# Kernel tuning notes

Hardware: AMD Instinct MI355X
Metric: run time of the kernel (lower is better)

Reference implementation:

```python
import jax, jax.numpy as jnp
import numpy as np

N_DATA = 131072
N_HID = 32768
D = 256
E1 = 524288  # data -> hidden
E2 = 524288  # hidden -> hidden
E3 = 524288  # hidden -> data


def setup_inputs() -> dict:
    key = jax.random.key(0)
    ks = jax.random.split(key, 32)
    rn = lambda k, shape, s=0.05: (jax.random.normal(k, shape, jnp.float32) * s)
    inp = {
        "data_x": jax.random.normal(ks[0], (N_DATA, 8), jnp.float32),
        "hidden_x": jax.random.normal(ks[1], (N_HID, 3), jnp.float32),
        "dh_src": jax.random.randint(ks[2], (E1,), 0, N_DATA, jnp.int32),
        "dh_dst": jax.random.randint(ks[3], (E1,), 0, N_HID, jnp.int32),
        "hh_src": jax.random.randint(ks[4], (E2,), 0, N_HID, jnp.int32),
        "hh_dst": jax.random.randint(ks[5], (E2,), 0, N_HID, jnp.int32),
        "hd_src": jax.random.randint(ks[6], (E3,), 0, N_HID, jnp.int32),
        "hd_dst": jax.random.randint(ks[7], (E3,), 0, N_DATA, jnp.int32),
        # encoder params
        "enc_src_w": rn(ks[8], (D, 8)), "enc_src_b": rn(ks[9], (D,)),
        "enc_dst_w": rn(ks[10], (D, 3)), "enc_dst_b": rn(ks[11], (D,)),
        "enc_wl": rn(ks[12], (D, D)), "enc_bl": rn(ks[13], (D,)), "enc_wr": rn(ks[14], (D, D)),
        # processor params
        "proc_wl": rn(ks[15], (D, D)), "proc_bl": rn(ks[16], (D,)), "proc_wr": rn(ks[17], (D, D)),
        "proc_mlp_w": rn(ks[18], (D, D)), "proc_mlp_b": rn(ks[19], (D,)),
        # decoder params
        "dec_src_w": rn(ks[20], (D, D)), "dec_src_b": rn(ks[21], (D,)),
        "dec_dst_w": rn(ks[22], (D, 8)), "dec_dst_b": rn(ks[23], (D,)),
        "dec_wl": rn(ks[24], (D, D)), "dec_bl": rn(ks[25], (D,)), "dec_wr": rn(ks[26], (D, D)),
        "out_w": rn(ks[27], (8, D)), "out_b": rn(ks[28], (8,)),
    }
    return inp


def _gelu(x):
    return jax.nn.gelu(x, approximate=False)  # torch nn.GELU default (erf)


def _sage(x_src, x_dst, src, dst, wl, bl, wr, n_dst):
    """PyG SAGEConv, mean aggregation: lin_l(mean_j x_src[j]) + lin_r(x_dst)."""
    msg = x_src[src]                                              # [E, D] gather
    agg = jax.ops.segment_sum(msg, dst, num_segments=n_dst)       # [n_dst, D]
    cnt = jax.ops.segment_sum(jnp.ones((src.shape[0], 1), msg.dtype), dst,
                              num_segments=n_dst)
    mean = agg / jnp.maximum(cnt, 1.0)
    return mean @ wl.T + bl + x_dst @ wr.T


def reference(data_x, hidden_x, dh_src, dh_dst, hh_src, hh_dst, hd_src, hd_dst,
              enc_src_w, enc_src_b, enc_dst_w, enc_dst_b, enc_wl, enc_bl, enc_wr,
              proc_wl, proc_bl, proc_wr, proc_mlp_w, proc_mlp_b,
              dec_src_w, dec_src_b, dec_dst_w, dec_dst_b, dec_wl, dec_bl, dec_wr,
              out_w, out_b):
    # ---- encoder: data -> hidden ----
    h_data = _gelu(data_x @ enc_src_w.T + enc_src_b)
    h_hid = _gelu(hidden_x @ enc_dst_w.T + enc_dst_b)
    h_hid = _gelu(_sage(h_data, h_hid, dh_src, dh_dst, enc_wl, enc_bl, enc_wr, N_HID))
    # ---- processor: hidden -> hidden, then GELU-Linear-GELU MLP ----
    h_hid = _sage(h_hid, h_hid, hh_src, hh_dst, proc_wl, proc_bl, proc_wr, N_HID)
    h_hid = _gelu(_gelu(h_hid) @ proc_mlp_w.T + proc_mlp_b)
    # ---- decoder: hidden -> data ----
    s = _gelu(h_hid @ dec_src_w.T + dec_src_b)
    d = _gelu(data_x @ dec_dst_w.T + dec_dst_b)
    d = _gelu(_sage(s, d, hd_src, hd_dst, dec_wl, dec_bl, dec_wr, N_DATA))
    return d @ out_w.T + out_b  # [N_DATA, 8]
```

## Files before the change

kernel.cpp:

```cpp
#include <hip/hip_runtime.h>
#include <stdint.h>

#define NDATA 131072
#define NHID  32768
#define NEDGE 524288

typedef __bf16 bf16_t;
typedef __bf16 bf16x4 __attribute__((ext_vector_type(4)));
typedef __bf16 bf16x8 __attribute__((ext_vector_type(8)));
typedef float  f32x4  __attribute__((ext_vector_type(4)));

__device__ __forceinline__ float gelu_f(float x) {
    return 0.5f * x * (1.0f + erff(x * 0.7071067811865476f));
}

__device__ __forceinline__ void glds16(const void* g, void* l) {
    auto* gp = reinterpret_cast<const __attribute__((address_space(1))) uint32_t*>(
        reinterpret_cast<uintptr_t>(g));
    auto* lp = reinterpret_cast<__attribute__((address_space(3))) uint32_t*>(
        reinterpret_cast<uintptr_t>(l));
    __builtin_amdgcn_global_load_lds(gp, lp, 16, 0, 0);
}

struct WPtrs { const float* p[9]; };

struct EdgePtrs { const int* src[3]; const int* dst[3]; };

__device__ __forceinline__ int cnt_off_of(int g) { return g == 0 ? 0 : (g == 1 ? NHID : 2 * NHID); }
__device__ __forceinline__ int rp_off_of(int g)  { return g == 0 ? 0 : (g == 1 ? NHID + 1 : 2 * NHID + 2); }
__device__ __forceinline__ int shift_of(int g)   { return g == 2 ? 10 : 8; }

__global__ __launch_bounds__(256)
void hist3(EdgePtrs ep, int* __restrict__ cnt_all) {
    const int g = blockIdx.x >> 11;
    const int i = ((blockIdx.x & 2047) << 8) + threadIdx.x;
    atomicAdd(&cnt_all[cnt_off_of(g) + ep.dst[g][i]], 1);
}

__global__ __launch_bounds__(256)
void scan_blk3(const int* __restrict__ cnt_all, int* __restrict__ pre_all,
               int* __restrict__ blk) {
    __shared__ int sh[256];
    const int bid = blockIdx.x;
    int g, local;
    if (bid < 32)      { g = 0; local = bid; }
    else if (bid < 64) { g = 1; local = bid - 32; }
    else               { g = 2; local = bid - 64; }
    const int t = threadIdx.x;
    const int cbase = cnt_off_of(g) + local * 1024 + t * 4;
    const int pbase = rp_off_of(g)  + local * 1024 + t * 4;
    int4 v = *(const int4*)(cnt_all + cbase);
    sh[t] = v.x + v.y + v.z + v.w;
    __syncthreads();
    for (int off = 1; off < 256; off <<= 1) {
        int other = 0;
        if (t >= off) other = sh[t - off];
        __syncthreads();
        if (t >= off) sh[t] += other;
        __syncthreads();
    }
    const int excl = (t == 0) ? 0 : sh[t - 1];
    int4 o;
    o.x = excl; o.y = o.x + v.x; o.z = o.y + v.y; o.w = o.z + v.z;
    *(int4*)(pre_all + pbase) = o;
    if (t == 255) blk[bid] = sh[255];
}

__global__ __launch_bounds__(256)
void scan_add3(const int* __restrict__ pre_all, const int* __restrict__ blk,
               int* __restrict__ rp_all, int* __restrict__ binA) {
    __shared__ int sh[256];
    const int bid = blockIdx.x;
    int g, local, gbase;
    if (bid < 32)      { g = 0; local = bid;      gbase = 0; }
    else if (bid < 64) { g = 1; local = bid - 32; gbase = 32; }
    else               { g = 2; local = bid - 64; gbase = 64; }
    const int t = threadIdx.x;
    int part = 0;
    if (t < local) part = blk[gbase + t];
    sh[t] = part;
    __syncthreads();
    for (int o2 = 128; o2 > 0; o2 >>= 1) {
        if (t < o2) sh[t] += sh[t + o2];
        __syncthreads();
    }
    const int off = sh[0];
    const int idx = local * 1024 + t * 4;
    const int pbase = rp_off_of(g) + idx;
    int4 v = *(const int4*)(pre_all + pbase);
    v.x += off; v.y += off; v.z += off; v.w += off;
    *(int4*)(rp_all + pbase) = v;
    const int bw = 1 << shift_of(g);
    if ((idx & (bw - 1)) == 0) binA[g * 128 + (idx >> shift_of(g))] = v.x;
    if (local == 0 && t == 0) {
        const int n = (g == 2) ? NDATA : NHID;
        rp_all[rp_off_of(g) + n] = NEDGE;
    }
}

__global__ __launch_bounds__(256)
void partition3(EdgePtrs ep, int* __restrict__ binA, int2* __restrict__ pairs) {
    __shared__ int hist[128], base[128], cur[128];
    const int g = blockIdx.x >> 7;
    const int blk = blockIdx.x & 127;
    const int t = threadIdx.x;
    const int shift = shift_of(g);
    const int e_base = blk * 4096;
    const int* src = ep.src[g];
    const int* dst = ep.dst[g];
    if (t < 128) { hist[t] = 0; cur[t] = 0; }
    __syncthreads();
    #pragma unroll
    for (int it = 0; it < 16; ++it) {
        const int d = dst[e_base + it * 256 + t];
        atomicAdd(&hist[d >> shift], 1);
    }
    __syncthreads();
    if (t < 128) base[t] = atomicAdd(&binA[g * 128 + t], hist[t]);
    __syncthreads();
    #pragma unroll
    for (int it = 0; it < 16; ++it) {
        const int e = e_base + it * 256 + t;
        const int s = src[e], d = dst[e];
        const int b = d >> shift;
        const int l = atomicAdd(&cur[b], 1);
        pairs[(size_t)g * NEDGE + base[b] + l] = make_int2(s, d);
    }
}

__global__ __launch_bounds__(256)
void binsort3(const int2* __restrict__ pairs, const int* __restrict__ rp_all,
              int* __restrict__ sorted_all) {
    __shared__ int cur[1024];
    const int g = blockIdx.x >> 7;
    const int b = blockIdx.x & 127;
    const int t = threadIdx.x;
    const int shift = shift_of(g);
    const int W = 1 << shift;
    const int d0 = b << shift;
    const int rpo = rp_off_of(g);
    for (int i = t; i < W; i += 256) cur[i] = rp_all[rpo + d0 + i];
    __syncthreads();
    const int e0 = rp_all[rpo + d0];
    const int e1 = rp_all[rpo + d0 + W];
    for (int e = e0 + t; e < e1; e += 256) {
        const int2 p = pairs[(size_t)g * NEDGE + e];
        const int pos = atomicAdd(&cur[p.y - d0], 1);
        sorted_all[(size_t)g * NEDGE + pos] = p.x;
    }
}

__global__ __launch_bounds__(256)
void csr_gather_mean(const bf16_t* __restrict__ feat, const int* __restrict__ row_ptr,
                     const int* __restrict__ sorted_src, bf16_t* __restrict__ mean, int n) {
    const int lane = threadIdx.x & 63;
    const int half = lane >> 5;
    const int col8 = (lane & 31) * 8;
    const int w = blockIdx.x * 4 + (threadIdx.x >> 6);
    if (w >= n) return;
    const int e0 = row_ptr[w], e1 = row_ptr[w + 1];
    float acc[8] = {0.f, 0.f, 0.f, 0.f, 0.f, 0.f, 0.f, 0.f};
    int e = e0 + half;
    for (; e + 6 < e1; e += 8) {
        const int s0 = sorted_src[e],     s1 = sorted_src[e + 2];
        const int s2 = sorted_src[e + 4], s3 = sorted_src[e + 6];
        const bf16x8 v0 = *(const bf16x8*)(feat + (size_t)s0 * 256 + col8);
        const bf16x8 v1 = *(const bf16x8*)(feat + (size_t)s1 * 256 + col8);
        const bf16x8 v2 = *(const bf16x8*)(feat + (size_t)s2 * 256 + col8);
        const bf16x8 v3 = *(const bf16x8*)(feat + (size_t)s3 * 256 + col8);
        #pragma unroll
        for (int j = 0; j < 8; ++j)
            acc[j] += ((float)v0[j] + (float)v1[j]) + ((float)v2[j] + (float)v3[j]);
    }
    for (; e < e1; e += 2) {
        const int s0 = sorted_src[e];
        const bf16x8 v0 = *(const bf16x8*)(feat + (size_t)s0 * 256 + col8);
        #pragma unroll
        for (int j = 0; j < 8; ++j) acc[j] += (float)v0[j];
    }
    #pragma unroll
    for (int j = 0; j < 8; ++j) acc[j] += __shfl_xor(acc[j], 32, 64);
    if (half == 0) {
        const float ic = 1.0f / fmaxf((float)(e1 - e0), 1.0f);
        bf16x8 r;
        #pragma unroll
        for (int j = 0; j < 8; ++j) r[j] = (bf16_t)(acc[j] * ic);
        *(bf16x8*)(mean + (size_t)w * 256 + col8) = r;
    }
}

__global__ __launch_bounds__(256)
void enc_cvt_both(WPtrs wp, bf16_t* __restrict__ wout,
                  const float* __restrict__ hx, const float* __restrict__ w3,
                  const float* __restrict__ b3, bf16_t* __restrict__ out3,
                  const float* __restrict__ dx, const float* __restrict__ w8,
                  const float* __restrict__ b8, bf16_t* __restrict__ out8) {
    __shared__ float ws[8 * 256];
    __shared__ float bs[256];
    const int t = threadIdx.x;
    if (blockIdx.x < 2056) {
        const int i = blockIdx.x * 256 + t;
        if (i < 8 * 65536) {
            const int wsel = i >> 16, off = i & 65535;
            wout[i] = (bf16_t)wp.p[wsel][off];
        } else {
            wout[i] = (bf16_t)wp.p[8][i - 8 * 65536];
        }
        return;
    }
    const int bid = blockIdx.x - 2056;
    const bool is8 = (bid >= 512);
    if (is8) {
        #pragma unroll
        for (int j = 0; j < 8; ++j) ws[j * 256 + t] = w8[t * 8 + j];
        bs[t] = b8[t];
    } else {
        #pragma unroll
        for (int j = 0; j < 3; ++j) ws[j * 256 + t] = w3[t * 3 + j];
        bs[t] = b3[t];
    }
    __syncthreads();
    const int lane = t & 63, wv = t >> 6;
    const int f0 = lane * 4;
    const float4 b4 = *(const float4*)(&bs[f0]);
    if (!is8) {
        for (int node = bid * 4 + wv; node < NHID; node += 512 * 4) {
            const float* xr = hx + (size_t)node * 3;
            float xv[3];
            #pragma unroll
            for (int j = 0; j < 3; ++j) xv[j] = xr[j];
            float a0 = b4.x, a1 = b4.y, a2 = b4.z, a3 = b4.w;
            #pragma unroll
            for (int j = 0; j < 3; ++j) {
                const float4 w4 = *(const float4*)(&ws[j * 256 + f0]);
                a0 += xv[j] * w4.x; a1 += xv[j] * w4.y;
                a2 += xv[j] * w4.z; a3 += xv[j] * w4.w;
            }
            bf16x4 r;
            r[0] = (bf16_t)gelu_f(a0); r[1] = (bf16_t)gelu_f(a1);
            r[2] = (bf16_t)gelu_f(a2); r[3] = (bf16_t)gelu_f(a3);
            *(bf16x4*)(out3 + (size_t)node * 256 + f0) = r;
        }
    } else {
        for (int node = (bid - 512) * 4 + wv; node < NDATA; node += 2048 * 4) {
            const float* xr = dx + (size_t)node * 8;
            float xv[8];
            #pragma unroll
            for (int j = 0; j < 8; ++j) xv[j] = xr[j];
            float a0 = b4.x, a1 = b4.y, a2 = b4.z, a3 = b4.w;
            #pragma unroll
            for (int j = 0; j < 8; ++j) {
                const float4 w4 = *(const float4*)(&ws[j * 256 + f0]);
                a0 += xv[j] * w4.x; a1 += xv[j] * w4.y;
                a2 += xv[j] * w4.z; a3 += xv[j] * w4.w;
            }
            bf16x4 r;
            r[0] = (bf16_t)gelu_f(a0); r[1] = (bf16_t)gelu_f(a1);
            r[2] = (bf16_t)gelu_f(a2); r[3] = (bf16_t)gelu_f(a3);
            *(bf16x4*)(out8 + (size_t)node * 256 + f0) = r;
        }
    }
}

template<int DUAL, int ACT>
__global__ __launch_bounds__(256)
void mfma_gemm(const bf16_t* __restrict__ A1, const bf16_t* __restrict__ W1,
               const bf16_t* __restrict__ A2, const bf16_t* __restrict__ W2,
               const float* __restrict__ bias, bf16_t* __restrict__ C) {
    __shared__ bf16_t As[4 * 64 * 8];
    __shared__ bf16_t Bs[4 * 128 * 8];
    const int t = threadIdx.x;
    const int w = t >> 6, lane = t & 63;
    const int l15 = lane & 15, l4 = lane >> 4;
    const int m0 = (blockIdx.x >> 1) * 64;
    const int n0 = (blockIdx.x & 1) * 128;

    f32x4 acc[4][2];
    #pragma unroll
    for (int nb = 0; nb < 2; ++nb) {
        const float bv = bias ? bias[n0 + w * 32 + nb * 16 + l15] : 0.0f;
        #pragma unroll
        for (int m = 0; m < 4; ++m) {
            acc[m][nb][0] = bv; acc[m][nb][1] = bv; acc[m][nb][2] = bv; acc[m][nb][3] = bv;
        }
    }

    #pragma unroll
    for (int p = 0; p <= DUAL; ++p) {
        const bf16_t* Ap = p ? A2 : A1;
        const bf16_t* Wp = p ? W2 : W1;
        for (int kt = 0; kt < 8; ++kt) {
            const int k0 = kt * 32;
            __syncthreads();
            glds16(Ap + (size_t)(m0 + lane) * 256 + k0 + w * 8, &As[(w * 64) * 8]);
            glds16(Wp + (size_t)(n0 + lane) * 256 + k0 + w * 8, &Bs[(w * 128) * 8]);
            glds16(Wp + (size_t)(n0 + 64 + lane) * 256 + k0 + w * 8, &Bs[(w * 128 + 64) * 8]);
            __syncthreads();
            bf16x8 af[4], bfr[2];
            #pragma unroll
            for (int m = 0; m < 4; ++m)
                af[m] = *(const bf16x8*)(&As[(l4 * 64 + m * 16 + l15) * 8]);
            #pragma unroll
            for (int nb = 0; nb < 2; ++nb)
                bfr[nb] = *(const bf16x8*)(&Bs[(l4 * 128 + w * 32 + nb * 16 + l15) * 8]);
            #pragma unroll
            for (int m = 0; m < 4; ++m)
                #pragma unroll
                for (int nb = 0; nb < 2; ++nb)
                    acc[m][nb] = __builtin_amdgcn_mfma_f32_16x16x32_bf16(af[m], bfr[nb], acc[m][nb], 0, 0, 0);
        }
    }

    #pragma unroll
    for (int m = 0; m < 4; ++m) {
        #pragma unroll
        for (int nb = 0; nb < 2; ++nb) {
            const int col = n0 + w * 32 + nb * 16 + l15;
            #pragma unroll
            for (int i = 0; i < 4; ++i) {
                const int row = m0 + m * 16 + l4 * 4 + i;
                const float v = acc[m][nb][i];
                C[(size_t)row * 256 + col] = (bf16_t)(ACT ? gelu_f(v) : v);
            }
        }
    }
}

__global__ __launch_bounds__(256)
void gemm_chain2(const bf16_t* __restrict__ A1, const bf16_t* __restrict__ W1,
                 const float* __restrict__ b1, const bf16_t* __restrict__ W2,
                 bf16_t* __restrict__ C) {
    __shared__ bf16_t As[4 * 64 * 8];
    __shared__ bf16_t Bs[4 * 256 * 8];
    __shared__ bf16_t sL[32 * 64 * 8];
    const int t = threadIdx.x;
    const int w = t >> 6, lane = t & 63;
    const int l15 = lane & 15, l4 = lane >> 4;
    const int m0 = blockIdx.x * 64;

    f32x4 acc[4][4];
    #pragma unroll
    for (int nb = 0; nb < 4; ++nb) {
        const float bv = b1[w * 64 + nb * 16 + l15];
        #pragma unroll
        for (int m = 0; m < 4; ++m) {
            acc[m][nb][0] = bv; acc[m][nb][1] = bv; acc[m][nb][2] = bv; acc[m][nb][3] = bv;
        }
    }

    for (int kt = 0; kt < 8; ++kt) {
        const int k0 = kt * 32;
        __syncthreads();
        glds16(A1 + (size_t)(m0 + lane) * 256 + k0 + w * 8, &As[(w * 64) * 8]);
        #pragma unroll
        for (int q = 0; q < 4; ++q)
            glds16(W1 + (size_t)(w * 64 + lane) * 256 + k0 + q * 8,
                   &Bs[(q * 256 + w * 64) * 8]);
        __syncthreads();
        bf16x8 af[4], bfr[4];
        #pragma unroll
        for (int m = 0; m < 4; ++m)
            af[m] = *(const bf16x8*)(&As[(l4 * 64 + m * 16 + l15) * 8]);
        #pragma unroll
        for (int nb = 0; nb < 4; ++nb)
            bfr[nb] = *(const bf16x8*)(&Bs[(l4 * 256 + w * 64 + nb * 16 + l15) * 8]);
        #pragma unroll
        for (int m = 0; m < 4; ++m)
            #pragma unroll
            for (int nb = 0; nb < 4; ++nb)
                acc[m][nb] = __builtin_amdgcn_mfma_f32_16x16x32_bf16(af[m], bfr[nb], acc[m][nb], 0, 0, 0);
    }
    #pragma unroll
    for (int m = 0; m < 4; ++m) {
        #pragma unroll
        for (int nb = 0; nb < 4; ++nb) {
            const int col = w * 64 + nb * 16 + l15;
            const int kq = col >> 3, cj = col & 7;
            #pragma unroll
            for (int i = 0; i < 4; ++i) {
                const int row = m * 16 + l4 * 4 + i;
                sL[(kq * 64 + row) * 8 + cj] = (bf16_t)gelu_f(acc[m][nb][i]);
            }
            acc[m][nb][0] = 0.f; acc[m][nb][1] = 0.f; acc[m][nb][2] = 0.f; acc[m][nb][3] = 0.f;
        }
    }
    __syncthreads();

    for (int kt = 0; kt < 8; ++kt) {
        const int k0 = kt * 32;
        __syncthreads();
        #pragma unroll
        for (int q = 0; q < 4; ++q)
            glds16(W2 + (size_t)(w * 64 + lane) * 256 + k0 + q * 8,
                   &Bs[(q * 256 + w * 64) * 8]);
        __syncthreads();
        bf16x8 af[4], bfr[4];
        #pragma unroll
        for (int m = 0; m < 4; ++m)
            af[m] = *(const bf16x8*)(&sL[((kt * 4 + l4) * 64 + m * 16 + l15) * 8]);
        #pragma unroll
        for (int nb = 0; nb < 4; ++nb)
            bfr[nb] = *(const bf16x8*)(&Bs[(l4 * 256 + w * 64 + nb * 16 + l15) * 8]);
        #pragma unroll
        for (int m = 0; m < 4; ++m)
            #pragma unroll
            for (int nb = 0; nb < 4; ++nb)
                acc[m][nb] = __builtin_amdgcn_mfma_f32_16x16x32_bf16(af[m], bfr[nb], acc[m][nb], 0, 0, 0);
    }

    #pragma unroll
    for (int m = 0; m < 4; ++m) {
        #pragma unroll
        for (int nb = 0; nb < 4; ++nb) {
            const int col = w * 64 + nb * 16 + l15;
            #pragma unroll
            for (int i = 0; i < 4; ++i) {
                const int row = m0 + m * 16 + l4 * 4 + i;
                C[(size_t)row * 256 + col] = (bf16_t)acc[m][nb][i];
            }
        }
    }
}

__global__ __launch_bounds__(256)
void dec_gemm_m(const bf16_t* __restrict__ A1mean,
                const float* __restrict__ xdat, const float* __restrict__ Wd,
                const float* __restrict__ bd, const bf16_t* __restrict__ W2,
                const float* __restrict__ bias, const bf16_t* __restrict__ owb,
                const float* __restrict__ ob, float* __restrict__ out) {
    __shared__ __align__(16) char smem[25600];
    bf16_t* As   = (bf16_t*)smem;
    bf16_t* Bs   = (bf16_t*)(smem + 4096);
    bf16_t* wd16 = (bf16_t*)(smem + 20480);
    float*  bdS  = (float*)(smem + 24576);
    bf16_t* tt   = (bf16_t*)smem;
    float*  part = (float*)(smem + 16384);

    const int t = threadIdx.x;
    const int w = t >> 6, lane = t & 63;
    const int l15 = lane & 15, l4 = lane >> 4;
    const int m0 = blockIdx.x * 64;

    {
        const float4 wa = *(const float4*)(Wd + t * 8);
        const float4 wb = *(const float4*)(Wd + t * 8 + 4);
        bf16x8 wv;
        wv[0] = (bf16_t)wa.x; wv[1] = (bf16_t)wa.y; wv[2] = (bf16_t)wa.z; wv[3] = (bf16_t)wa.w;
        wv[4] = (bf16_t)wb.x; wv[5] = (bf16_t)wb.y; wv[6] = (bf16_t)wb.z; wv[7] = (bf16_t)wb.w;
        *(bf16x8*)(&wd16[t * 8]) = wv;
        bdS[t] = bd[t];
    }
    bf16x8 af_x;
    #pragma unroll
    for (int j = 0; j < 8; ++j) af_x[j] = (bf16_t)0.0f;
    if (l4 == 0) {
        const float* xrp = xdat + (size_t)(m0 + w * 16 + l15) * 8;
        const float4 xa = *(const float4*)(xrp);
        const float4 xb = *(const float4*)(xrp + 4);
        af_x[0] = (bf16_t)xa.x; af_x[1] = (bf16_t)xa.y; af_x[2] = (bf16_t)xa.z; af_x[3] = (bf16_t)xa.w;
        af_x[4] = (bf16_t)xb.x; af_x[5] = (bf16_t)xb.y; af_x[6] = (bf16_t)xb.z; af_x[7] = (bf16_t)xb.w;
    }

    f32x4 acc[4][4];
    #pragma unroll
    for (int nb = 0; nb < 4; ++nb) {
        const float bv = bias[w * 64 + nb * 16 + l15];
        #pragma unroll
        for (int m = 0; m < 4; ++m) {
            acc[m][nb][0] = bv; acc[m][nb][1] = bv; acc[m][nb][2] = bv; acc[m][nb][3] = bv;
        }
    }
    {
        bf16x8 ifr[2];
        #pragma unroll
        for (int p = 0; p < 2; ++p)
            #pragma unroll
            for (int j = 0; j < 8; ++j)
                ifr[p][j] = (bf16_t)((l4 * 8 + j == p * 16 + l15) ? 1.0f : 0.0f);
        #pragma unroll
        for (int m = 0; m < 4; ++m) {
            #pragma unroll
            for (int c = 0; c < 2; ++c) {
                const bf16x8 am = *(const bf16x8*)(A1mean +
                    (size_t)(m0 + m * 16 + l15) * 256 + (2 * w + c) * 32 + l4 * 8);
                acc[m][c * 2 + 0] = __builtin_amdgcn_mfma_f32_16x16x32_bf16(am, ifr[0], acc[m][c * 2 + 0], 0, 0, 0);
                acc[m][c * 2 + 1] = __builtin_amdgcn_mfma_f32_16x16x32_bf16(am, ifr[1], acc[m][c * 2 + 1], 0, 0, 0);
            }
        }
    }
    __syncthreads();

    for (int kt = 0; kt < 8; ++kt) {
        const int k0 = kt * 32;
        __syncthreads();
        #pragma unroll
        for (int nb2 = 0; nb2 < 2; ++nb2) {
            const int cl = nb2 * 16 + l15;
            const int col = k0 + cl;
            f32x4 ad;
            const float bv = bdS[col];
            ad[0] = bv; ad[1] = bv; ad[2] = bv; ad[3] = bv;
            bf16x8 bf_d;
            #pragma unroll
            for (int j = 0; j < 8; ++j) bf_d[j] = (bf16_t)0.0f;
            if (l4 == 0) bf_d = *(const bf16x8*)(&wd16[col * 8]);
            ad = __builtin_amdgcn_mfma_f32_16x16x32_bf16(af_x, bf_d, ad, 0, 0, 0);
            const int kq = cl >> 3, jj = cl & 7;
            #pragma unroll
            for (int i = 0; i < 4; ++i)
                As[(kq * 64 + w * 16 + l4 * 4 + i) * 8 + jj] = (bf16_t)gelu_f(ad[i]);
        }
        #pragma unroll
        for (int q = 0; q < 4; ++q)
            glds16(W2 + (size_t)(w * 64 + lane) * 256 + k0 + q * 8,
                   &Bs[(q * 256 + w * 64) * 8]);
        __syncthreads();
        bf16x8 af[4], bfr[4];
        #pragma unroll
        for (int m = 0; m < 4; ++m)
            af[m] = *(const bf16x8*)(&As[(l4 * 64 + m * 16 + l15) * 8]);
        #pragma unroll
        for (int nb = 0; nb < 4; ++nb)
            bfr[nb] = *(const bf16x8*)(&Bs[(l4 * 256 + w * 64 + nb * 16 + l15) * 8]);
        #pragma unroll
        for (int m = 0; m < 4; ++m)
            #pragma unroll
            for (int nb = 0; nb < 4; ++nb)
                acc[m][nb] = __builtin_amdgcn_mfma_f32_16x16x32_bf16(af[m], bfr[nb], acc[m][nb], 0, 0, 0);
    }

    __syncthreads();

    bf16x8 owf[2];
    #pragma unroll
    for (int s = 0; s < 2; ++s) {
        #pragma unroll
        for (int j = 0; j < 8; ++j) owf[s][j] = (bf16_t)0.0f;
        if (l15 < 8)
            owf[s] = *(const bf16x8*)(owb + l15 * 256 + w * 64 + s * 32 + l4 * 8);
    }

    bf16_t* ttw = tt + w * 2048;
    #pragma unroll
    for (int h = 0; h < 2; ++h) {
        #pragma unroll
        for (int mm = 0; mm < 2; ++mm) {
            const int m = h * 2 + mm;
            #pragma unroll
            for (int nb = 0; nb < 4; ++nb) {
                const int col = nb * 16 + l15;
                const int kg = col >> 3, cj = col & 7;
                #pragma unroll
                for (int i = 0; i < 4; ++i) {
                    const int rl = mm * 16 + l4 * 4 + i;
                    ttw[(kg * 32 + rl) * 8 + cj] = (bf16_t)gelu_f(acc[m][nb][i]);
                }
            }
        }
        f32x4 accp[2];
        #pragma unroll
        for (int mb = 0; mb < 2; ++mb) {
            accp[mb][0] = 0.f; accp[mb][1] = 0.f; accp[mb][2] = 0.f; accp[mb][3] = 0.f;
            #pragma unroll
            for (int s = 0; s < 2; ++s) {
                const bf16x8 af = *(const bf16x8*)(&ttw[((s * 4 + l4) * 32 + mb * 16 + l15) * 8]);
                accp[mb] = __builtin_amdgcn_mfma_f32_16x16x32_bf16(af, owf[s], accp[mb], 0, 0, 0);
            }
        }
        __syncthreads();
        #pragma unroll
        for (int mb = 0; mb < 2; ++mb)
            #pragma unroll
            for (int i = 0; i < 4; ++i)
                part[(w * 32 + mb * 16 + l4 * 4 + i) * 16 + l15] = accp[mb][i];
        __syncthreads();
        {
            const int row = t >> 3, o = t & 7;
            const float v = part[(0 * 32 + row) * 16 + o] + part[(1 * 32 + row) * 16 + o]
                          + part[(2 * 32 + row) * 16 + o] + part[(3 * 32 + row) * 16 + o] + ob[o];
            out[(size_t)(m0 + h * 32 + row) * 8 + o] = v;
        }
    }
}


extern "C" void kernel_launch(void* const* d_in, const int* in_sizes, int n_in,
                              void* d_out, int out_size, void* d_ws, size_t ws_size,
                              hipStream_t stream) {
    const float* data_x   = (const float*)d_in[0];
    const float* hidden_x = (const float*)d_in[1];
    const int* dh_src = (const int*)d_in[2];
    const int* dh_dst = (const int*)d_in[3];
    const int* hh_src = (const int*)d_in[4];
    const int* hh_dst = (const int*)d_in[5];
    const int* hd_src = (const int*)d_in[6];
    const int* hd_dst = (const int*)d_in[7];
    const float* enc_src_w = (const float*)d_in[8];
    const float* enc_src_b = (const float*)d_in[9];
    const float* enc_dst_w = (const float*)d_in[10];
    const float* enc_dst_b = (const float*)d_in[11];
    const float* enc_wl = (const float*)d_in[12];
    const float* enc_bl = (const float*)d_in[13];
    const float* enc_wr = (const float*)d_in[14];
    const float* proc_wl = (const float*)d_in[15];
    const float* proc_bl = (const float*)d_in[16];
    const float* proc_wr = (const float*)d_in[17];
    const float* proc_mlp_w = (const float*)d_in[18];
    const float* proc_mlp_b = (const float*)d_in[19];
    const float* dec_src_w = (const float*)d_in[20];
    const float* dec_src_b = (const float*)d_in[21];
    const float* dec_dst_w = (const float*)d_in[22];
    const float* dec_dst_b = (const float*)d_in[23];
    const float* dec_wl = (const float*)d_in[24];
    const float* dec_bl = (const float*)d_in[25];
    const float* dec_wr = (const float*)d_in[26];
    const float* out_w  = (const float*)d_in[27];
    const float* out_b  = (const float*)d_in[28];
    float* out = (float*)d_out;

    bf16_t* h_a   = (bf16_t*)d_ws;
    bf16_t* h_b   = h_a + (size_t)NHID * 256;
    bf16_t* h_c   = h_b + (size_t)NHID * 256;
    bf16_t* h_msg = h_c + (size_t)NHID * 256;
    bf16_t* dmean = h_msg + (size_t)NDATA * 256;
    bf16_t* wbuf  = dmean + (size_t)NDATA * 256;
    int* cnt_all    = (int*)(wbuf + 8 * 65536 + 2048);
    int* rp_all     = cnt_all + (2 * NHID + NDATA);
    int* sorted_all = rp_all + (2 * NHID + NDATA + 3);
    int* blk_sums   = sorted_all + (size_t)3 * NEDGE;
    int* binA       = blk_sums + 192;
    int2* pairs     = (int2*)(((uintptr_t)(binA + 384) + 15) & ~(uintptr_t)15);

    bf16_t* W_enc_wl  = wbuf + 0 * 65536;
    bf16_t* W_enc_wr  = wbuf + 1 * 65536;
    bf16_t* W_proc_wl = wbuf + 2 * 65536;
    bf16_t* W_proc_wr = wbuf + 3 * 65536;
    bf16_t* W_mlp     = wbuf + 4 * 65536;
    bf16_t* W_dec_src = wbuf + 5 * 65536;
    bf16_t* W_dec_wl  = wbuf + 6 * 65536;
    bf16_t* W_dec_wr  = wbuf + 7 * 65536;
    bf16_t* W_out     = wbuf + 8 * 65536;

    const int* rp_dh = rp_all;
    const int* rp_hh = rp_all + NHID + 1;
    const int* rp_hd = rp_all + 2 * NHID + 2;
    const int* so_dh = sorted_all;
    const int* so_hh = sorted_all + NEDGE;
    const int* so_hd = sorted_all + 2 * (size_t)NEDGE;

    WPtrs wp;
    wp.p[0] = enc_wl;  wp.p[1] = enc_wr;  wp.p[2] = proc_wl; wp.p[3] = proc_wr;
    wp.p[4] = proc_mlp_w; wp.p[5] = dec_src_w; wp.p[6] = dec_wl; wp.p[7] = dec_wr;
    wp.p[8] = out_w;

    EdgePtrs ep;
    ep.src[0] = dh_src; ep.dst[0] = dh_dst;
    ep.src[1] = hh_src; ep.dst[1] = hh_dst;
    ep.src[2] = hd_src; ep.dst[2] = hd_dst;
    hipMemsetAsync(cnt_all, 0, (size_t)(2 * NHID + NDATA) * sizeof(int), stream);
    hist3<<<3 * 2048, 256, 0, stream>>>(ep, cnt_all);
    scan_blk3<<<192, 256, 0, stream>>>(cnt_all, rp_all, blk_sums);
    scan_add3<<<192, 256, 0, stream>>>(rp_all, blk_sums, rp_all, binA);
    partition3<<<3 * 128, 256, 0, stream>>>(ep, binA, pairs);
    binsort3<<<3 * 128, 256, 0, stream>>>(pairs, rp_all, sorted_all);

    enc_cvt_both<<<4616, 256, 0, stream>>>(wp, wbuf,
                                           hidden_x, enc_dst_w, enc_dst_b, h_a,
                                           data_x, enc_src_w, enc_src_b, h_msg);
    csr_gather_mean<<<NHID / 4, 256, 0, stream>>>(h_msg, rp_dh, so_dh, h_b, NHID);
    mfma_gemm<1, 1><<<(NHID / 64) * 2, 256, 0, stream>>>(h_b, W_enc_wl, h_a, W_enc_wr, enc_bl, h_c);

    csr_gather_mean<<<NHID / 4, 256, 0, stream>>>(h_c, rp_hh, so_hh, h_a, NHID);
    mfma_gemm<1, 1><<<(NHID / 64) * 2, 256, 0, stream>>>(h_a, W_proc_wl, h_c, W_proc_wr, proc_bl, h_b);
    mfma_gemm<0, 1><<<(NHID / 64) * 2, 256, 0, stream>>>(h_b, W_mlp, nullptr, nullptr, proc_mlp_b, h_a);
    gemm_chain2<<<NHID / 64, 256, 0, stream>>>(h_a, W_dec_src, dec_src_b, W_dec_wl, h_c);

    csr_gather_mean<<<NDATA / 4, 256, 0, stream>>>(h_c, rp_hd, so_hd, dmean, NDATA);
    dec_gemm_m<<<NDATA / 64, 256, 0, stream>>>(dmean, data_x, dec_dst_w, dec_dst_b,
                                               W_dec_wr, dec_bl, W_out, out_b, out);
}
```

Before: 448.3 us.

## Precompute decoder dst tile in LDS and read W2 fragments from global

Result: no change. 454.9 us (+1.5%).

```diff
diff --git a/kernel.cpp b/kernel.cpp
--- a/kernel.cpp
+++ b/kernel.cpp
@@ -22,7 +22,7 @@
     __builtin_amdgcn_global_load_lds(gp, lp, 16, 0, 0);
 }
 
-struct WPtrs { const float* p[9]; };
+struct WPtrs { const float* p[10]; };
 
 struct EdgePtrs { const int* src[3]; const int* dst[3]; };
 
@@ -198,17 +198,19 @@
     __shared__ float ws[8 * 256];
     __shared__ float bs[256];
     const int t = threadIdx.x;
-    if (blockIdx.x < 2056) {
+    if (blockIdx.x < 2064) {
         const int i = blockIdx.x * 256 + t;
         if (i < 8 * 65536) {
             const int wsel = i >> 16, off = i & 65535;
             wout[i] = (bf16_t)wp.p[wsel][off];
+        } else if (i < 8 * 65536 + 2048) {
+            wout[i] = (bf16_t)wp.p[8][i - 8 * 65536];
         } else {
-            wout[i] = (bf16_t)wp.p[8][i - 8 * 65536];
+            wout[i] = (bf16_t)wp.p[9][i - (8 * 65536 + 2048)];
         }
         return;
     }
-    const int bid = blockIdx.x - 2056;
+    const int bid = blockIdx.x - 2064;
     const bool is8 = (bid >= 512);
     if (is8) {
         #pragma unroll
@@ -424,15 +426,12 @@
 
 __global__ __launch_bounds__(256)
 void dec_gemm_m(const bf16_t* __restrict__ A1mean,
-                const float* __restrict__ xdat, const float* __restrict__ Wd,
+                const float* __restrict__ xdat, const bf16_t* __restrict__ wdb,
                 const float* __restrict__ bd, const bf16_t* __restrict__ W2,
                 const float* __restrict__ bias, const bf16_t* __restrict__ owb,
                 const float* __restrict__ ob, float* __restrict__ out) {
-    __shared__ __align__(16) char smem[25600];
-    bf16_t* As   = (bf16_t*)smem;
-    bf16_t* Bs   = (bf16_t*)(smem + 4096);
-    bf16_t* wd16 = (bf16_t*)(smem + 20480);
-    float*  bdS  = (float*)(smem + 24576);
+    __shared__ __align__(16) char smem[32768];
+    bf16_t* dL = (bf16_t*)smem;
     bf16_t* tt   = (bf16_t*)smem;
     float*  part = (float*)(smem + 16384);
 
@@ -441,15 +440,6 @@
     const int l15 = lane & 15, l4 = lane >> 4;
     const int m0 = blockIdx.x * 64;
 
-    {
-        const float4 wa = *(const float4*)(Wd + t * 8);
-        const float4 wb = *(const float4*)(Wd + t * 8 + 4);
-        bf16x8 wv;
-        wv[0] = (bf16_t)wa.x; wv[1] = (bf16_t)wa.y; wv[2] = (bf16_t)wa.z; wv[3] = (bf16_t)wa.w;
-        wv[4] = (bf16_t)wb.x; wv[5] = (bf16_t)wb.y; wv[6] = (bf16_t)wb.z; wv[7] = (bf16_t)wb.w;
-        *(bf16x8*)(&wd16[t * 8]) = wv;
-        bdS[t] = bd[t];
-    }
     bf16x8 af_x;
     #pragma unroll
     for (int j = 0; j < 8; ++j) af_x[j] = (bf16_t)0.0f;
@@ -461,6 +451,23 @@
         af_x[4] = (bf16_t)xb.x; af_x[5] = (bf16_t)xb.y; af_x[6] = (bf16_t)xb.z; af_x[7] = (bf16_t)xb.w;
     }
 
+    #pragma unroll
+    for (int cb = 0; cb < 16; ++cb) {
+        const int col = cb * 16 + l15;
+        f32x4 ad;
+        const float bv = bd[col];
+        ad[0] = bv; ad[1] = bv; ad[2] = bv; ad[3] = bv;
+        bf16x8 bf_d;
+        #pragma unroll
+        for (int j = 0; j < 8; ++j) bf_d[j] = (bf16_t)0.0f;
+        if (l4 == 0) bf_d = *(const bf16x8*)(wdb + col * 8);
+        ad = __builtin_amdgcn_mfma_f32_16x16x32_bf16(af_x, bf_d, ad, 0, 0, 0);
+        const int kq = col >> 3, jj = col & 7;
+        #pragma unroll
+        for (int i = 0; i < 4; ++i)
+            dL[(kq * 64 + w * 16 + l4 * 4 + i) * 8 + jj] = (bf16_t)gelu_f(ad[i]);
+    }
+
     f32x4 acc[4][4];
     #pragma unroll
     for (int nb = 0; nb < 4; ++nb) {
@@ -492,36 +499,14 @@
 
     for (int kt = 0; kt < 8; ++kt) {
         const int k0 = kt * 32;
-        __syncthreads();
-        #pragma unroll
-        for (int nb2 = 0; nb2 < 2; ++nb2) {
-            const int cl = nb2 * 16 + l15;
-            const int col = k0 + cl;
-            f32x4 ad;
-            const float bv = bdS[col];
-            ad[0] = bv; ad[1] = bv; ad[2] = bv; ad[3] = bv;
-            bf16x8 bf_d;
-            #pragma unroll
-            for (int j = 0; j < 8; ++j) bf_d[j] = (bf16_t)0.0f;
-            if (l4 == 0) bf_d = *(const bf16x8*)(&wd16[col * 8]);
-            ad = __builtin_amdgcn_mfma_f32_16x16x32_bf16(af_x, bf_d, ad, 0, 0, 0);
-            const int kq = cl >> 3, jj = cl & 7;
-            #pragma unroll
-            for (int i = 0; i < 4; ++i)
-                As[(kq * 64 + w * 16 + l4 * 4 + i) * 8 + jj] = (bf16_t)gelu_f(ad[i]);
-        }
-        #pragma unroll
-        for (int q = 0; q < 4; ++q)
-            glds16(W2 + (size_t)(w * 64 + lane) * 256 + k0 + q * 8,
-                   &Bs[(q * 256 + w * 64) * 8]);
-        __syncthreads();
-        bf16x8 af[4], bfr[4];
+        bf16x8 bfr[4];
+        #pragma unroll
+        for (int nb = 0; nb < 4; ++nb)
+            bfr[nb] = *(const bf16x8*)(W2 + (size_t)(w * 64 + nb * 16 + l15) * 256 + k0 + l4 * 8);
+        bf16x8 af[4];
         #pragma unroll
         for (int m = 0; m < 4; ++m)
-            af[m] = *(const bf16x8*)(&As[(l4 * 64 + m * 16 + l15) * 8]);
-        #pragma unroll
-        for (int nb = 0; nb < 4; ++nb)
-            bfr[nb] = *(const bf16x8*)(&Bs[(l4 * 256 + w * 64 + nb * 16 + l15) * 8]);
+            af[m] = *(const bf16x8*)(&dL[((kt * 4 + l4) * 64 + m * 16 + l15) * 8]);
         #pragma unroll
         for (int m = 0; m < 4; ++m)
             #pragma unroll
@@ -624,7 +609,7 @@
     bf16_t* h_msg = h_c + (size_t)NHID * 256;
     bf16_t* dmean = h_msg + (size_t)NDATA * 256;
     bf16_t* wbuf  = dmean + (size_t)NDATA * 256;
-    int* cnt_all    = (int*)(wbuf + 8 * 65536 + 2048);
+    int* cnt_all    = (int*)(wbuf + 8 * 65536 + 4096);
     int* rp_all     = cnt_all + (2 * NHID + NDATA);
     int* sorted_all = rp_all + (2 * NHID + NDATA + 3);
     int* blk_sums   = sorted_all + (size_t)3 * NEDGE;
@@ -640,6 +625,7 @@
     bf16_t* W_dec_wl  = wbuf + 6 * 65536;
     bf16_t* W_dec_wr  = wbuf + 7 * 65536;
     bf16_t* W_out     = wbuf + 8 * 65536;
+    bf16_t* W_dd      = wbuf + 8 * 65536 + 2048;
 
     const int* rp_dh = rp_all;
     const int* rp_hh = rp_all + NHID + 1;
@@ -651,7 +637,7 @@
     WPtrs wp;
     wp.p[0] = enc_wl;  wp.p[1] = enc_wr;  wp.p[2] = proc_wl; wp.p[3] = proc_wr;
     wp.p[4] = proc_mlp_w; wp.p[5] = dec_src_w; wp.p[6] = dec_wl; wp.p[7] = dec_wr;
-    wp.p[8] = out_w;
+    wp.p[8] = out_w; wp.p[9] = dec_dst_w;
 
     EdgePtrs ep;
     ep.src[0] = dh_src; ep.dst[0] = dh_dst;
@@ -664,7 +650,7 @@
     partition3<<<3 * 128, 256, 0, stream>>>(ep, binA, pairs);
     binsort3<<<3 * 128, 256, 0, stream>>>(pairs, rp_all, sorted_all);
 
-    enc_cvt_both<<<4616, 256, 0, stream>>>(wp, wbuf,
+    enc_cvt_both<<<4624, 256, 0, stream>>>(wp, wbuf,
                                            hidden_x, enc_dst_w, enc_dst_b, h_a,
                                            data_x, enc_src_w, enc_src_b, h_msg);
     csr_gather_mean<<<NHID / 4, 256, 0, stream>>>(h_msg, rp_dh, so_dh, h_b, NHID);
@@ -676,6 +662,6 @@
     gemm_chain2<<<NHID / 64, 256, 0, stream>>>(h_a, W_dec_src, dec_src_b, W_dec_wl, h_c);
 
     csr_gather_mean<<<NDATA / 4, 256, 0, stream>>>(h_c, rp_hd, so_hd, dmean, NDATA);
-    dec_gemm_m<<<NDATA / 64, 256, 0, stream>>>(dmean, data_x, dec_dst_w, dec_dst_b,
+    dec_gemm_m<<<NDATA / 64, 256, 0, stream>>>(dmean, data_x, W_dd, dec_dst_b,
                                                W_dec_wr, dec_bl, W_out, out_b, out);
 }
```
